# Performance work log

Hardware: AMD Instinct MI355X
Metric: run time of the kernel (lower is better)

## Reference

```python
import jax, jax.numpy as jnp
import numpy as np

B, H, S, DH = 1, 16, 4096, 128
D_MODEL = H * DH  # 2048


def setup_inputs() -> dict:
    key = jax.random.key(0)
    kq, kk, kv = jax.random.split(key, 3)
    q = jax.random.normal(kq, (B, H, S, DH), dtype=jnp.float32)
    k = jax.random.normal(kk, (B, H, S, DH), dtype=jnp.float32)
    v = jax.random.normal(kv, (B, H, S, DH), dtype=jnp.float32)
    # causal mask: 1 where attending is allowed, 0 elsewhere (masked_fill on ==0)
    attn_mask = jnp.tril(jnp.ones((S, S), dtype=jnp.int32))[None, None, :, :]
    return {"q": q, "k": k, "v": v, "seq_length": S, "attn_mask": attn_mask}


def reference(q, k, v, seq_length, attn_mask):
    # q,k,v: [1, H, S, DH]; attn_mask: [1, 1, S, S] (0 = masked)
    scale = 1.0 / jnp.sqrt(jnp.asarray(q.shape[-1], dtype=q.dtype))
    att = jnp.einsum("bhqd,bhkd->bhqk", q, k) * scale  # [1,H,S,S]
    mask = attn_mask[:, :, :seq_length, :seq_length]
    att = jnp.where(mask == 0, jnp.asarray(-jnp.inf, dtype=att.dtype), att)
    att = jax.nn.softmax(att, axis=-1)
    y = jnp.einsum("bhqk,bhkd->bhqd", att, v)  # [1,H,S,DH]
    # transpose(1,2) -> [1,S,H,DH] -> view(S, d_model)
    y = jnp.transpose(y, (0, 2, 1, 3)).reshape(seq_length, H * DH)
    return y
```

## Files before the change

### kernel.cpp

```cpp
#include <hip/hip_runtime.h>

#define HH 16
#define SS 4096
#define DHD 128
#define BC 64
#define LDK 144
#define LDV 68
#define LDPT 72
#define DM (HH * DHD)

#define OFF_K   0
#define OFF_VT  18432
#define OFF_PT  35840
#define SMEM_SZ 45056

typedef __bf16 bf16x8_t __attribute__((ext_vector_type(8)));
typedef __bf16 bf16x4_t __attribute__((ext_vector_type(4)));
typedef float  f32x4_t  __attribute__((ext_vector_type(4)));

#define BAR() asm volatile("s_waitcnt lgkmcnt(0)\n\ts_barrier" ::: "memory")

__device__ __forceinline__ f32x4_t vmax4(f32x4_t a, f32x4_t b) {
    f32x4_t r;
    r[0] = fmaxf(a[0], b[0]); r[1] = fmaxf(a[1], b[1]);
    r[2] = fmaxf(a[2], b[2]); r[3] = fmaxf(a[3], b[3]);
    return r;
}

__global__ __launch_bounds__(256, 3)
void fa_fwd(const float* __restrict__ q, const float* __restrict__ k,
            const float* __restrict__ v, float* __restrict__ out)
{
    const int b  = blockIdx.x;
    const int qt = 63 - (b >> 4);
    const int h  = b & 15;
    const int J  = qt + 1;

    const int tid  = threadIdx.x;
    const int wave = tid >> 6;
    const int lane = tid & 63;
    const int l16  = lane & 15;
    const int quad = lane >> 4;
    const int rK   = tid >> 5;
    const int c4   = tid & 31;
    const int dbase = (wave & 1) * 64;
    const int rbase = (wave >> 1) * 32;

    __shared__ __align__(16) char smem[SMEM_SZ];
    unsigned short* k_s  = (unsigned short*)(smem + OFF_K);
    unsigned short* vt_s = (unsigned short*)(smem + OFF_VT);
    unsigned short* pT_s = (unsigned short*)(smem + OFF_PT);

    const size_t hoff = (size_t)h * SS * DHD;
    const float* qh = q + hoff;
    const float* kh = k + hoff;
    const float* vh = v + hoff;

    const float scale = 0.088388347648318447f * 1.4426950408889634f;

    float4 kreg[8];
    float  vreg[8][4];
    auto issue = [&](int j) {
        const float* kb = kh + (size_t)j * BC * DHD;
        #pragma unroll
        for (int i = 0; i < 8; ++i)
            kreg[i] = ((const float4*)(kb + (size_t)(rK + i * 8) * DHD))[c4];
        const float* vb = vh + (size_t)j * BC * DHD + dbase + lane;
        #pragma unroll
        for (int p = 0; p < 8; ++p) {
            const float* vp = vb + (size_t)(rbase + p * 4) * DHD;
            vreg[p][0] = vp[0];
            vreg[p][1] = vp[DHD];
            vreg[p][2] = vp[2 * DHD];
            vreg[p][3] = vp[3 * DHD];
        }
    };

    issue(0);

    bf16x8_t qf[4];
    {
        const float* qb = qh + (size_t)(qt * 64 + wave * 16 + l16) * DHD;
        #pragma unroll
        for (int kc = 0; kc < 4; ++kc) {
            const float* row = qb + kc * 32 + quad * 8;
            float4 a0 = *(const float4*)row;
            float4 a1 = *(const float4*)(row + 4);
            bf16x8_t f;
            f[0] = (__bf16)(a0.x * scale); f[1] = (__bf16)(a0.y * scale);
            f[2] = (__bf16)(a0.z * scale); f[3] = (__bf16)(a0.w * scale);
            f[4] = (__bf16)(a1.x * scale); f[5] = (__bf16)(a1.y * scale);
            f[6] = (__bf16)(a1.z * scale); f[7] = (__bf16)(a1.w * scale);
            qf[kc] = f;
        }
    }

    f32x4_t oacc[8];
    #pragma unroll
    for (int mt = 0; mt < 8; ++mt) oacc[mt] = (f32x4_t)(0.0f);
    float mi = -INFINITY, li = 0.0f;
    const int q_local = wave * 16 + l16;

    for (int j = 0; j < J; ++j) {
        BAR();
        #pragma unroll
        for (int i = 0; i < 8; ++i) {
            bf16x4_t bb;
            bb[0] = (__bf16)kreg[i].x; bb[1] = (__bf16)kreg[i].y;
            bb[2] = (__bf16)kreg[i].z; bb[3] = (__bf16)kreg[i].w;
            *(bf16x4_t*)&k_s[(rK + i * 8) * LDK + c4 * 4] = bb;
        }
        #pragma unroll
        for (int p = 0; p < 8; ++p) {
            bf16x4_t bb;
            bb[0] = (__bf16)vreg[p][0]; bb[1] = (__bf16)vreg[p][1];
            bb[2] = (__bf16)vreg[p][2]; bb[3] = (__bf16)vreg[p][3];
            *(bf16x4_t*)&vt_s[(dbase + lane) * LDV + rbase + p * 4] = bb;
        }
        if (j + 1 < J) issue(j + 1);
        BAR();

        f32x4_t sa[4];
        #pragma unroll
        for (int mt = 0; mt < 4; ++mt) sa[mt] = (f32x4_t)(0.0f);
        #pragma unroll
        for (int kc = 0; kc < 4; ++kc)
            #pragma unroll
            for (int mt = 0; mt < 4; ++mt) {
                bf16x8_t kf = *(const bf16x8_t*)
                    &k_s[(mt * 16 + l16) * LDK + kc * 32 + quad * 8];
                sa[mt] = __builtin_amdgcn_mfma_f32_16x16x32_bf16(kf, qf[kc], sa[mt], 0, 0, 0);
            }

        if (j == qt) {
            #pragma unroll
            for (int mt = 0; mt < 4; ++mt)
                #pragma unroll
                for (int r = 0; r < 4; ++r)
                    if (mt * 16 + quad * 4 + r > q_local) sa[mt][r] = -INFINITY;
        }

        f32x4_t mv = vmax4(vmax4(sa[0], sa[1]), vmax4(sa[2], sa[3]));
        float mx = fmaxf(fmaxf(mv[0], mv[1]), fmaxf(mv[2], mv[3]));
        mx = fmaxf(mx, __shfl_xor(mx, 16));
        mx = fmaxf(mx, __shfl_xor(mx, 32));
        float mnew = fmaxf(mi, mx);
        float a = exp2f(mi - mnew);
        mi = mnew;
        bf16x4_t pkv[4];
        #pragma unroll
        for (int mt = 0; mt < 4; ++mt) {
            #pragma unroll
            for (int r = 0; r < 4; ++r) sa[mt][r] = exp2f(sa[mt][r] - mnew);
            pkv[mt][0] = (__bf16)sa[mt][0]; pkv[mt][1] = (__bf16)sa[mt][1];
            pkv[mt][2] = (__bf16)sa[mt][2]; pkv[mt][3] = (__bf16)sa[mt][3];
        }
        f32x4_t sv = (sa[0] + sa[1]) + (sa[2] + sa[3]);
        float rs = (sv[0] + sv[1]) + (sv[2] + sv[3]);
        rs += __shfl_xor(rs, 16);
        rs += __shfl_xor(rs, 32);
        li = li * a + rs;

        #pragma unroll
        for (int mt = 0; mt < 4; ++mt)
            *(bf16x4_t*)&pT_s[(wave * 16 + l16) * LDPT + mt * 16 + quad * 4] = pkv[mt];

        #pragma unroll
        for (int mt = 0; mt < 8; ++mt) {
            oacc[mt][0] *= a; oacc[mt][1] *= a;
            oacc[mt][2] *= a; oacc[mt][3] *= a;
        }

        #pragma unroll
        for (int kc = 0; kc < 2; ++kc) {
            bf16x8_t pb = *(const bf16x8_t*)
                &pT_s[(wave * 16 + l16) * LDPT + kc * 32 + quad * 8];
            #pragma unroll
            for (int mt = 0; mt < 8; ++mt) {
                bf16x4_t vlo = *(const bf16x4_t*)
                    &vt_s[(mt * 16 + l16) * LDV + kc * 32 + quad * 8];
                bf16x4_t vhi = *(const bf16x4_t*)
                    &vt_s[(mt * 16 + l16) * LDV + kc * 32 + quad * 8 + 4];
                bf16x8_t vf = __builtin_shufflevector(vlo, vhi, 0,1,2,3,4,5,6,7);
                oacc[mt] = __builtin_amdgcn_mfma_f32_16x16x32_bf16(vf, pb, oacc[mt], 0, 0, 0);
            }
        }
    }

    float iv = 1.0f / li;
    float* op = out + (size_t)(qt * 64 + wave * 16 + l16) * DM + h * DHD;
    #pragma unroll
    for (int mt = 0; mt < 8; ++mt) {
        f32x4_t vv = oacc[mt];
        vv[0] *= iv; vv[1] *= iv; vv[2] *= iv; vv[3] *= iv;
        *(f32x4_t*)&op[mt * 16 + quad * 4] = vv;
    }
}

extern "C" void kernel_launch(void* const* d_in, const int* in_sizes, int n_in,
                              void* d_out, int out_size, void* d_ws, size_t ws_size,
                              hipStream_t stream) {
    const float* q = (const float*)d_in[0];
    const float* k = (const float*)d_in[1];
    const float* v = (const float*)d_in[2];
    float* out = (float*)d_out;
    fa_fwd<<<dim3((SS / 64) * HH), dim3(256), 0, stream>>>(q, k, v, out);
}
```

Before: 320.9 us.

## Pair causal query tiles per block and double-buffer K/V in LDS

Each block now processes two query tiles, g and 63-g, back to back, so every block does the same 65 KV iterations and the causal triangle is load-balanced. The grid is halved to 512 blocks. K/V LDS staging is double-buffered, which leaves one barrier per iteration, with the global prefetch issued two tiles ahead. This roughly doubles LDS use and lowers the occupancy hint from 3 to 2 blocks per CU, so latency hiding across blocks is reduced.

```diff
diff --git a/kernel.cpp b/kernel.cpp
--- a/kernel.cpp
+++ b/kernel.cpp
@@ -9,10 +9,12 @@
 #define LDPT 72
 #define DM (HH * DHD)
 
-#define OFF_K   0
-#define OFF_VT  18432
-#define OFF_PT  35840
-#define SMEM_SZ 45056
+#define OFF_K0  0
+#define OFF_K1  18432
+#define OFF_VT0 36864
+#define OFF_VT1 54272
+#define OFF_PT  71680
+#define SMEM_SZ 80896
 
 typedef __bf16 bf16x8_t __attribute__((ext_vector_type(8)));
 typedef __bf16 bf16x4_t __attribute__((ext_vector_type(4)));
@@ -27,14 +29,16 @@
     return r;
 }
 
-__global__ __launch_bounds__(256, 3)
+__global__ __launch_bounds__(256, 2)
 void fa_fwd(const float* __restrict__ q, const float* __restrict__ k,
             const float* __restrict__ v, float* __restrict__ out)
 {
-    const int b  = blockIdx.x;
-    const int qt = 63 - (b >> 4);
-    const int h  = b & 15;
-    const int J  = qt + 1;
+    const int b   = blockIdx.x;
+    const int h   = b & 15;
+    const int g   = b >> 4;
+    const int qt0 = g, qt1 = 63 - g;
+    const int n0  = g + 1;
+    const int J   = 65;
 
     const int tid  = threadIdx.x;
     const int wave = tid >> 6;
@@ -47,8 +51,6 @@
     const int rbase = (wave >> 1) * 32;
 
     __shared__ __align__(16) char smem[SMEM_SZ];
-    unsigned short* k_s  = (unsigned short*)(smem + OFF_K);
-    unsigned short* vt_s = (unsigned short*)(smem + OFF_VT);
     unsigned short* pT_s = (unsigned short*)(smem + OFF_PT);
 
     const size_t hoff = (size_t)h * SS * DHD;
@@ -75,11 +77,28 @@
             vreg[p][3] = vp[3 * DHD];
         }
     };
-
-    issue(0);
+    auto commit = [&](int buf) {
+        unsigned short* kd = (unsigned short*)(smem + (buf ? OFF_K1 : OFF_K0));
+        unsigned short* vd = (unsigned short*)(smem + (buf ? OFF_VT1 : OFF_VT0));
+        #pragma unroll
+        for (int i = 0; i < 8; ++i) {
+            bf16x4_t bb;
+            bb[0] = (__bf16)kreg[i].x; bb[1] = (__bf16)kreg[i].y;
+            bb[2] = (__bf16)kreg[i].z; bb[3] = (__bf16)kreg[i].w;
+            *(bf16x4_t*)&kd[(rK + i * 8) * LDK + c4 * 4] = bb;
+        }
+        #pragma unroll
+        for (int p = 0; p < 8; ++p) {
+            bf16x4_t bb;
+            bb[0] = (__bf16)vreg[p][0]; bb[1] = (__bf16)vreg[p][1];
+            bb[2] = (__bf16)vreg[p][2]; bb[3] = (__bf16)vreg[p][3];
+            *(bf16x4_t*)&vd[(dbase + lane) * LDV + rbase + p * 4] = bb;
+        }
+    };
+    auto jof = [&](int i) { return i < n0 ? i : i - n0; };
 
     bf16x8_t qf[4];
-    {
+    auto loadQ = [&](int qt) {
         const float* qb = qh + (size_t)(qt * 64 + wave * 16 + l16) * DHD;
         #pragma unroll
         for (int kc = 0; kc < 4; ++kc) {
@@ -93,32 +112,50 @@
             f[6] = (__bf16)(a1.z * scale); f[7] = (__bf16)(a1.w * scale);
             qf[kc] = f;
         }
-    }
+    };
 
     f32x4_t oacc[8];
-    #pragma unroll
-    for (int mt = 0; mt < 8; ++mt) oacc[mt] = (f32x4_t)(0.0f);
-    float mi = -INFINITY, li = 0.0f;
-    const int q_local = wave * 16 + l16;
-
-    for (int j = 0; j < J; ++j) {
-        BAR();
-        #pragma unroll
-        for (int i = 0; i < 8; ++i) {
-            bf16x4_t bb;
-            bb[0] = (__bf16)kreg[i].x; bb[1] = (__bf16)kreg[i].y;
-            bb[2] = (__bf16)kreg[i].z; bb[3] = (__bf16)kreg[i].w;
-            *(bf16x4_t*)&k_s[(rK + i * 8) * LDK + c4 * 4] = bb;
-        }
-        #pragma unroll
-        for (int p = 0; p < 8; ++p) {
-            bf16x4_t bb;
-            bb[0] = (__bf16)vreg[p][0]; bb[1] = (__bf16)vreg[p][1];
-            bb[2] = (__bf16)vreg[p][2]; bb[3] = (__bf16)vreg[p][3];
-            *(bf16x4_t*)&vt_s[(dbase + lane) * LDV + rbase + p * 4] = bb;
-        }
-        if (j + 1 < J) issue(j + 1);
-        BAR();
+    float mi, li;
+    auto resetAcc = [&]() {
+        #pragma unroll
+        for (int mt = 0; mt < 8; ++mt) oacc[mt] = (f32x4_t)(0.0f);
+        mi = -INFINITY; li = 0.0f;
+    };
+    auto storeTile = [&](int qt) {
+        float iv = 1.0f / li;
+        float* op = out + (size_t)(qt * 64 + wave * 16 + l16) * DM + h * DHD;
+        #pragma unroll
+        for (int mt = 0; mt < 8; ++mt) {
+            f32x4_t vv = oacc[mt];
+            vv[0] *= iv; vv[1] *= iv; vv[2] *= iv; vv[3] *= iv;
+            *(f32x4_t*)&op[mt * 16 + quad * 4] = vv;
+        }
+    };
+
+    issue(jof(0));
+    commit(0);
+    issue(jof(1));
+    loadQ(qt0);
+    resetAcc();
+    BAR();
+
+    for (int i = 0; i < J; ++i) {
+        const int t   = (i >= n0);
+        const int qtc = t ? qt1 : qt0;
+        const int j   = t ? i - n0 : i;
+        if (i == n0) {
+            storeTile(qt0);
+            resetAcc();
+            loadQ(qt1);
+        }
+
+        if (i + 1 < J) commit((i + 1) & 1);
+        if (i + 2 < J) issue(jof(i + 2));
+
+        const unsigned short* k_s  =
+            (const unsigned short*)(smem + ((i & 1) ? OFF_K1 : OFF_K0));
+        const unsigned short* vt_s =
+            (const unsigned short*)(smem + ((i & 1) ? OFF_VT1 : OFF_VT0));
 
         f32x4_t sa[4];
         #pragma unroll
@@ -132,12 +169,13 @@
                 sa[mt] = __builtin_amdgcn_mfma_f32_16x16x32_bf16(kf, qf[kc], sa[mt], 0, 0, 0);
             }
 
-        if (j == qt) {
+        if (j == qtc) {
+            const int ql = wave * 16 + l16;
             #pragma unroll
             for (int mt = 0; mt < 4; ++mt)
                 #pragma unroll
                 for (int r = 0; r < 4; ++r)
-                    if (mt * 16 + quad * 4 + r > q_local) sa[mt][r] = -INFINITY;
+                    if (mt * 16 + quad * 4 + r > ql) sa[mt][r] = -INFINITY;
         }
 
         f32x4_t mv = vmax4(vmax4(sa[0], sa[1]), vmax4(sa[2], sa[3]));
@@ -185,16 +223,10 @@
                 oacc[mt] = __builtin_amdgcn_mfma_f32_16x16x32_bf16(vf, pb, oacc[mt], 0, 0, 0);
             }
         }
+        BAR();
     }
 
-    float iv = 1.0f / li;
-    float* op = out + (size_t)(qt * 64 + wave * 16 + l16) * DM + h * DHD;
-    #pragma unroll
-    for (int mt = 0; mt < 8; ++mt) {
-        f32x4_t vv = oacc[mt];
-        vv[0] *= iv; vv[1] *= iv; vv[2] *= iv; vv[3] *= iv;
-        *(f32x4_t*)&op[mt * 16 + quad * 4] = vv;
-    }
+    storeTile(qt1);
 }
 
 extern "C" void kernel_launch(void* const* d_in, const int* in_sizes, int n_in,
@@ -204,5 +236,5 @@
     const float* k = (const float*)d_in[1];
     const float* v = (const float*)d_in[2];
     float* out = (float*)d_out;
-    fa_fwd<<<dim3((SS / 64) * HH), dim3(256), 0, stream>>>(q, k, v, out);
+    fa_fwd<<<dim3((SS / 128) * HH), dim3(256), 0, stream>>>(q, k, v, out);
 }
```

Result: faster. 307.6 us (-4.1%).
